# Kernel optimization log

Measured on AMD Instinct MI355X. Metric: run time of the kernel, lower is better.

## Reference

```python
import jax, jax.numpy as jnp
import numpy as np

BIT_DEPTH = 8  # feature squeezing

def setup_inputs() -> dict:
    key = jax.random.key(0)
    ks = jax.random.split(key, 8)
    B, C, H, W = 8, 256, 64, 64
    Cq = C // 8
    x = jax.random.normal(ks[0], (B, C, H, W), dtype=jnp.float32)
    # 1x1 conv weights stored as [out, in] (kernel dims squeezed)
    wq = jax.random.normal(ks[1], (Cq, C), dtype=jnp.float32) * 0.05
    bq = jax.random.normal(ks[2], (Cq,), dtype=jnp.float32) * 0.05
    wk = jax.random.normal(ks[3], (Cq, C), dtype=jnp.float32) * 0.05
    bk = jax.random.normal(ks[4], (Cq,), dtype=jnp.float32) * 0.05
    wv = jax.random.normal(ks[5], (C, C), dtype=jnp.float32) * 0.05
    bv = jax.random.normal(ks[6], (C,), dtype=jnp.float32) * 0.05
    gamma = jax.random.normal(ks[7], (1,), dtype=jnp.float32) * 0.1
    return {"x": x, "wq": wq, "bq": bq, "wk": wk, "bk": bk, "wv": wv, "bv": bv, "gamma": gamma}

def reference(x, wq, bq, wk, bk, wv, bv, gamma):
    B, C, H, W = x.shape
    N = H * W
    xf = x.reshape(B, C, N)  # flatten spatial
    # 1x1 convs == per-pixel linear projections
    q = jnp.einsum('bcn,oc->bon', xf, wq) + bq[None, :, None]   # [B, C/8, N]
    k = jnp.einsum('bcn,oc->bon', xf, wk) + bk[None, :, None]   # [B, C/8, N]
    v = jnp.einsum('bcn,oc->bon', xf, wv) + bv[None, :, None]   # [B, C, N]
    energy = jnp.einsum('bcn,bcm->bnm', q, k)                   # [B, N, N] (no scaling, as in source)
    attn = jax.nn.softmax(energy, axis=-1)
    out = jnp.einsum('bcm,bnm->bcn', v, attn).reshape(B, C, H, W)
    out = gamma[0] * out + out               # gamma-scaled residual of attention output
    scale = jnp.float32(2 ** BIT_DEPTH)
    return jnp.floor(out * scale) / scale    # feature squeezing (bit_depth=8)
```

## Files before the change

kernel.cpp:

```cpp
#include <hip/hip_runtime.h>
#include <math.h>

namespace {
constexpr int BB = 8;
constexpr int CH = 256;
constexpr int NN = 4096;
}

typedef float f32x4 __attribute__((ext_vector_type(4)));
typedef short bf16x8 __attribute__((ext_vector_type(8)));
typedef unsigned short us8 __attribute__((ext_vector_type(8)));

#define MFMA16(a, b, c) __builtin_amdgcn_mfma_f32_16x16x32_bf16(a, b, c, 0, 0, 0)

__device__ __forceinline__ unsigned short f2bf(float x) {
    unsigned int u = __float_as_uint(x);
    u += 0x7fffu + ((u >> 16) & 1u);
    return (unsigned short)(u >> 16);
}
__device__ __forceinline__ float bf2f(unsigned short h) {
    return __uint_as_float(((unsigned int)h) << 16);
}
__device__ __forceinline__ void gload16(const void* g, void* l) {
    __builtin_amdgcn_global_load_lds(
        (const __attribute__((address_space(1))) unsigned int*)g,
        (__attribute__((address_space(3))) unsigned int*)l, 16, 0, 0);
}

__global__ __launch_bounds__(256) void wsplit_kernel(
    const float* __restrict__ wq, const float* __restrict__ wk,
    const float* __restrict__ wv,
    unsigned short* __restrict__ wh, unsigned short* __restrict__ wl)
{
    int idx = blockIdx.x * 256 + threadIdx.x;
    float v;
    if (idx < 8192)       v = wq[idx];
    else if (idx < 16384) v = wk[idx - 8192];
    else                  v = wv[idx - 16384];
    unsigned short hi = f2bf(v);
    wh[idx] = hi;
    wl[idx] = f2bf(v - bf2f(hi));
}

#define PJ_XH 0
#define PJ_XL 32768
#define PJ_ST 65536
#define PJ_QK 65536
#define PJ_VE 0

__global__ __launch_bounds__(256, 2) void proj_kernel(
    const float* __restrict__ x,
    const unsigned short* __restrict__ wh, const unsigned short* __restrict__ wl,
    const float* __restrict__ bq, const float* __restrict__ bk,
    const float* __restrict__ bv,
    unsigned short* __restrict__ qh, unsigned short* __restrict__ ql,
    unsigned short* __restrict__ kh, unsigned short* __restrict__ kl,
    unsigned short* __restrict__ vt)
{
    __shared__ __align__(16) unsigned char smem[81920];
    const int t    = threadIdx.x;
    const int lane = t & 63;
    const int w    = t >> 6;
    const int l16  = lane & 15;
    const int quad = lane >> 4;
    const int b    = blockIdx.x >> 6;
    const int n0   = (blockIdx.x & 63) << 6;

    const unsigned char* xB = (const unsigned char*)x + ((size_t)b * 256 * NN + n0) * 4;
    const int n = t & 63;
    #pragma unroll 1
    for (int cg = 0; cg < 4; ++cg) {
        __syncthreads();
        #pragma unroll
        for (int j = 0; j < 4; ++j) {
            int idx = j * 256 + t;
            int cr = idx >> 4, nch = idx & 15;
            gload16(xB + (size_t)(cg * 64 + cr) * NN * 4 + nch * 16,
                    smem + PJ_ST + idx * 16);
        }
        __syncthreads();
        #pragma unroll
        for (int it = 0; it < 2; ++it) {
            int o = (t >> 6) + 4 * it;
            us8 h8, l8;
            #pragma unroll
            for (int j = 0; j < 8; ++j) {
                float v = *(const float*)(smem + PJ_ST + (o * 8 + j) * 256 + n * 4);
                unsigned short hi = f2bf(v);
                h8[j] = hi;
                l8[j] = f2bf(v - bf2f(hi));
            }
            int pch = (cg * 8 + o) ^ (n & 7);
            *(us8*)(smem + PJ_XH + n * 512 + pch * 16) = h8;
            *(us8*)(smem + PJ_XL + n * 512 + pch * 16) = l8;
        }
    }
    __syncthreads();

    f32x4 acc[5][4] = {};
    #pragma unroll 1
    for (int kc = 0; kc < 8; ++kc) {
        bf16x8 ah[5], al[5];
        #pragma unroll
        for (int i = 0; i < 5; ++i) {
            int och = (w * 5 + i) * 16 + l16;
            ah[i] = *(const bf16x8*)(wh + och * 256 + kc * 32 + quad * 8);
            al[i] = *(const bf16x8*)(wl + och * 256 + kc * 32 + quad * 8);
        }
        #pragma unroll
        for (int nt = 0; nt < 4; ++nt) {
            int roff = (nt * 16 + l16) * 512 + (((kc * 4 + quad) ^ (l16 & 7)) * 16);
            bf16x8 bh = *(const bf16x8*)(smem + PJ_XH + roff);
            bf16x8 bl = *(const bf16x8*)(smem + PJ_XL + roff);
            #pragma unroll
            for (int i = 0; i < 5; ++i) {
                acc[i][nt] = MFMA16(ah[i], bh, acc[i][nt]);
                acc[i][nt] = MFMA16(al[i], bh, acc[i][nt]);
                acc[i][nt] = MFMA16(ah[i], bl, acc[i][nt]);
            }
        }
    }
    __syncthreads();

    #pragma unroll
    for (int i = 0; i < 5; ++i) {
        int tile = w * 5 + i;
        if (tile < 4) {
            #pragma unroll
            for (int r = 0; r < 4; ++r) {
                int och = tile * 16 + quad * 4 + r;
                float bias = (och < 32) ? bq[och] : bk[och - 32];
                int arr = (och < 32) ? 0 : 2;
                int oq = och & 31;
                #pragma unroll
                for (int nt = 0; nt < 4; ++nt) {
                    float val = acc[i][nt][r] + bias;
                    unsigned short hi = f2bf(val);
                    unsigned short lo = f2bf(val - bf2f(hi));
                    *(unsigned short*)(smem + PJ_QK + arr * 4096 + (nt * 16 + l16) * 64 + oq * 2) = hi;
                    *(unsigned short*)(smem + PJ_QK + (arr + 1) * 4096 + (nt * 16 + l16) * 64 + oq * 2) = lo;
                }
            }
        } else {
            #pragma unroll
            for (int r = 0; r < 4; ++r) {
                int voch = tile * 16 + quad * 4 + r - 64;
                float bias = bv[voch];
                #pragma unroll
                for (int nt = 0; nt < 4; ++nt) {
                    *(unsigned short*)(smem + PJ_VE + voch * 136 + (nt * 16 + l16) * 2)
                        = f2bf(acc[i][nt][r] + bias);
                }
            }
        }
    }
    __syncthreads();

    {
        unsigned short* dsts[4] = { qh, ql, kh, kl };
        int arr = t >> 6, rn = t & 63;
        unsigned short* dst = dsts[arr] + ((size_t)b * NN + n0 + rn) * 32;
        #pragma unroll
        for (int i = 0; i < 4; ++i)
            *(us8*)(dst + i * 8) = *(const us8*)(smem + PJ_QK + arr * 4096 + rn * 64 + i * 16);
    }
    #pragma unroll
    for (int p = 0; p < 4; ++p) {
        int voch = p * 64 + (t >> 2), piece = t & 3;
        unsigned short* dst = vt + ((size_t)b * CH + voch) * NN + n0 + piece * 16;
        *(us8*)(dst)     = *(const us8*)(smem + PJ_VE + voch * 136 + piece * 32);
        *(us8*)(dst + 8) = *(const us8*)(smem + PJ_VE + voch * 136 + piece * 32 + 16);
    }
}

#define AV_OFF 0
#define AK_OFF 49152
#define AP_OFF 61440
#define AS_OFF 71680

__global__ __launch_bounds__(256, 2) void attn_kernel(
    const unsigned short* __restrict__ qh, const unsigned short* __restrict__ ql,
    const unsigned short* __restrict__ kh, const unsigned short* __restrict__ kl,
    const unsigned short* __restrict__ vt, const float* __restrict__ gptr,
    float* __restrict__ out)
{
    __shared__ __align__(16) unsigned char smem[71936];
    const int t    = threadIdx.x;
    const int lane = t & 63;
    const int w    = t >> 6;
    const int l16  = lane & 15;
    const int quad = lane >> 4;
    const int b    = blockIdx.x & 7;
    const int n0   = (blockIdx.x >> 3) << 6;

    const size_t qrow = (size_t)b * NN + n0 + w * 16 + l16;
    const bf16x8 qhA = *(const bf16x8*)(qh + qrow * 32 + quad * 8);
    const bf16x8 qlA = *(const bf16x8*)(ql + qrow * 32 + quad * 8);

    const unsigned char* ksrc;
    int kdst;
    {
        int c = t & 127, kr = c >> 2, cl = c & 3;
        int cg = cl ^ ((kr >> 1) & 3);
        ksrc = (const unsigned char*)((t < 128) ? kh : kl)
             + (size_t)b * NN * 64 + (size_t)kr * 64 + cg * 16;
        kdst = AK_OFF + (t >> 7) * 2048 + c * 16;
    }
    const unsigned char* vsrc;
    {
        int vr = t >> 2, cl = t & 3;
        int cg = cl ^ (vr & 3);
        vsrc = (const unsigned char*)vt + (size_t)b * CH * NN * 2
             + (size_t)vr * 8192 + cg * 16;
    }

    f32x4 acc[4][4] = {};
    float S[4] = {};

    {
        gload16(ksrc, smem + kdst);
        unsigned char* vd = smem + AV_OFF + t * 16;
        gload16(vsrc,           vd);
        gload16(vsrc + 524288,  vd + 4096);
        gload16(vsrc + 1048576, vd + 8192);
        gload16(vsrc + 1572864, vd + 12288);
    }
    __syncthreads();

    int bprv = 2, bcur = 0, bnxt = 1, pcur = 0;
    const int koffbase = (quad ^ ((l16 >> 1) & 3)) * 16;
    const int voffbase = (quad ^ (l16 & 3)) * 16;

    #pragma unroll 1
    for (int r = 0; r < 128; ++r) {
        if (r < 127) {
            const unsigned char* ks = ksrc + (size_t)(r + 1) * 2048;
            gload16(ks, smem + bnxt * 4096 + kdst);
            const unsigned char* vs = vsrc + (size_t)(r + 1) * 64;
            unsigned char* vd = smem + AV_OFF + bnxt * 16384 + t * 16;
            gload16(vs,           vd);
            gload16(vs + 524288,  vd + 4096);
            gload16(vs + 1048576, vd + 8192);
            gload16(vs + 1572864, vd + 12288);
        }
        {
            const unsigned char* kb = smem + AK_OFF + bcur * 4096;
            unsigned char* pb = smem + AP_OFF + pcur * 5120;
            #pragma unroll
            for (int kt = 0; kt < 2; ++kt) {
                int ko = (kt * 16 + l16) * 64 + koffbase;
                bf16x8 bh = *(const bf16x8*)(kb + ko);
                bf16x8 bl = *(const bf16x8*)(kb + 2048 + ko);
                f32x4 e = { 0.f, 0.f, 0.f, 0.f };
                e = MFMA16(qhA, bh, e);
                e = MFMA16(qlA, bh, e);
                e = MFMA16(qhA, bl, e);
                #pragma unroll
                for (int rr = 0; rr < 4; ++rr) {
                    float p = __expf(e[rr]);
                    unsigned short pv16 = f2bf(p);
                    S[rr] += bf2f(pv16);
                    *(unsigned short*)(pb + (w * 16 + quad * 4 + rr) * 80
                                          + (kt * 16 + l16) * 2) = pv16;
                }
            }
        }
        if (r > 0) {
            const unsigned char* pp = smem + AP_OFF + (pcur ^ 1) * 5120;
            const unsigned char* vb = smem + AV_OFF + bprv * 16384;
            bf16x8 aP[4], bV[4];
            #pragma unroll
            for (int qt = 0; qt < 4; ++qt)
                aP[qt] = *(const bf16x8*)(pp + (qt * 16 + l16) * 80 + quad * 16);
            #pragma unroll
            for (int ct = 0; ct < 4; ++ct)
                bV[ct] = *(const bf16x8*)(vb + (w * 64 + ct * 16 + l16) * 64 + voffbase);
            #pragma unroll
            for (int qt = 0; qt < 4; ++qt)
                #pragma unroll
                for (int ct = 0; ct < 4; ++ct)
                    acc[qt][ct] = MFMA16(aP[qt], bV[ct], acc[qt][ct]);
        }
        __syncthreads();
        bprv = bcur; bcur = bnxt; ++bnxt; if (bnxt == 3) bnxt = 0;
        pcur ^= 1;
    }
    {
        const unsigned char* pp = smem + AP_OFF + (pcur ^ 1) * 5120;
        const unsigned char* vb = smem + AV_OFF + bprv * 16384;
        bf16x8 aP[4], bV[4];
        #pragma unroll
        for (int qt = 0; qt < 4; ++qt)
            aP[qt] = *(const bf16x8*)(pp + (qt * 16 + l16) * 80 + quad * 16);
        #pragma unroll
        for (int ct = 0; ct < 4; ++ct)
            bV[ct] = *(const bf16x8*)(vb + (w * 64 + ct * 16 + l16) * 64 + voffbase);
        #pragma unroll
        for (int qt = 0; qt < 4; ++qt)
            #pragma unroll
            for (int ct = 0; ct < 4; ++ct)
                acc[qt][ct] = MFMA16(aP[qt], bV[ct], acc[qt][ct]);
    }

    #pragma unroll
    for (int mask = 1; mask <= 8; mask <<= 1)
        #pragma unroll
        for (int rr = 0; rr < 4; ++rr)
            S[rr] += __shfl_xor(S[rr], mask);
    float* SM = (float*)(smem + AS_OFF);
    __syncthreads();
    if (l16 == 0) {
        #pragma unroll
        for (int rr = 0; rr < 4; ++rr)
            SM[w * 16 + quad * 4 + rr] = S[rr];
    }
    __syncthreads();

    const float g1 = 1.f + gptr[0];
    float* ob = out + (size_t)b * CH * NN;
    #pragma unroll
    for (int qt = 0; qt < 4; ++qt) {
        float is[4];
        #pragma unroll
        for (int rr = 0; rr < 4; ++rr)
            is[rr] = g1 / SM[qt * 16 + quad * 4 + rr];
        #pragma unroll
        for (int ct = 0; ct < 4; ++ct) {
            float4 o4;
            o4.x = floorf(acc[qt][ct][0] * is[0] * 256.f) * 0.00390625f;
            o4.y = floorf(acc[qt][ct][1] * is[1] * 256.f) * 0.00390625f;
            o4.z = floorf(acc[qt][ct][2] * is[2] * 256.f) * 0.00390625f;
            o4.w = floorf(acc[qt][ct][3] * is[3] * 256.f) * 0.00390625f;
            *(float4*)(ob + (size_t)(w * 64 + ct * 16 + l16) * NN
                          + n0 + qt * 16 + quad * 4) = o4;
        }
    }
}

extern "C" void kernel_launch(void* const* d_in, const int* in_sizes, int n_in,
                              void* d_out, int out_size, void* d_ws, size_t ws_size,
                              hipStream_t stream) {
    const float* x  = (const float*)d_in[0];
    const float* wq = (const float*)d_in[1];
    const float* bq = (const float*)d_in[2];
    const float* wk = (const float*)d_in[3];
    const float* bk = (const float*)d_in[4];
    const float* wv = (const float*)d_in[5];
    const float* bv = (const float*)d_in[6];
    const float* gm = (const float*)d_in[7];
    float* out = (float*)d_out;

    unsigned short* ws = (unsigned short*)d_ws;
    const size_t WSZ = 320 * 256;
    const size_t QSZ = (size_t)BB * NN * 32;
    unsigned short* wh = ws;
    unsigned short* wl = wh + WSZ;
    unsigned short* qh = wl + WSZ;
    unsigned short* ql = qh + QSZ;
    unsigned short* kh = ql + QSZ;
    unsigned short* kl = kh + QSZ;
    unsigned short* vt = kl + QSZ;

    wsplit_kernel<<<320, 256, 0, stream>>>(wq, wk, wv, wh, wl);
    proj_kernel<<<512, 256, 0, stream>>>(x, wh, wl, bq, bk, bv,
                                         qh, ql, kh, kl, vt);
    attn_kernel<<<512, 256, 0, stream>>>(qh, ql, kh, kl, vt, gm, out);
}
```

Baseline: 246.9 us.

## Load K and V fragments straight to registers instead of staging through LDS

The attention kernel no longer copies K and V tiles into shared memory with async global-to-LDS loads. Each wave now reads its K fragment (16 keys) and V fragments directly from global memory into registers, double-buffered across iterations. Key tiles grow to 64 per iteration and each wave computes scores for all 64 queries, with partial row sums combined through shared memory at the end. The projection kernel likewise loads x with vectorized global reads into registers instead of LDS staging, shrinking shared memory. The intent is to cut LDS traffic and footprint to allow higher occupancy, at the cost of more registers and less coalesced, uncached direct global loads of V.

```diff
diff --git a/kernel.cpp b/kernel.cpp
--- a/kernel.cpp
+++ b/kernel.cpp
@@ -20,11 +20,6 @@
 }
 __device__ __forceinline__ float bf2f(unsigned short h) {
     return __uint_as_float(((unsigned int)h) << 16);
-}
-__device__ __forceinline__ void gload16(const void* g, void* l) {
-    __builtin_amdgcn_global_load_lds(
-        (const __attribute__((address_space(1))) unsigned int*)g,
-        (__attribute__((address_space(3))) unsigned int*)l, 16, 0, 0);
 }
 
 __global__ __launch_bounds__(256) void wsplit_kernel(
@@ -44,9 +39,8 @@
 
 #define PJ_XH 0
 #define PJ_XL 32768
-#define PJ_ST 65536
-#define PJ_QK 65536
 #define PJ_VE 0
+#define PJ_QK 36864
 
 __global__ __launch_bounds__(256, 2) void proj_kernel(
     const float* __restrict__ x,
@@ -57,7 +51,7 @@
     unsigned short* __restrict__ kh, unsigned short* __restrict__ kl,
     unsigned short* __restrict__ vt)
 {
-    __shared__ __align__(16) unsigned char smem[81920];
+    __shared__ __align__(16) unsigned char smem[65536];
     const int t    = threadIdx.x;
     const int lane = t & 63;
     const int w    = t >> 6;
@@ -66,33 +60,26 @@
     const int b    = blockIdx.x >> 6;
     const int n0   = (blockIdx.x & 63) << 6;
 
-    const unsigned char* xB = (const unsigned char*)x + ((size_t)b * 256 * NN + n0) * 4;
-    const int n = t & 63;
-    #pragma unroll 1
-    for (int cg = 0; cg < 4; ++cg) {
-        __syncthreads();
-        #pragma unroll
-        for (int j = 0; j < 4; ++j) {
-            int idx = j * 256 + t;
-            int cr = idx >> 4, nch = idx & 15;
-            gload16(xB + (size_t)(cg * 64 + cr) * NN * 4 + nch * 16,
-                    smem + PJ_ST + idx * 16);
-        }
-        __syncthreads();
-        #pragma unroll
-        for (int it = 0; it < 2; ++it) {
-            int o = (t >> 6) + 4 * it;
-            us8 h8, l8;
-            #pragma unroll
-            for (int j = 0; j < 8; ++j) {
-                float v = *(const float*)(smem + PJ_ST + (o * 8 + j) * 256 + n * 4);
-                unsigned short hi = f2bf(v);
-                h8[j] = hi;
-                l8[j] = f2bf(v - bf2f(hi));
-            }
-            int pch = (cg * 8 + o) ^ (n & 7);
-            *(us8*)(smem + PJ_XH + n * 512 + pch * 16) = h8;
-            *(us8*)(smem + PJ_XL + n * 512 + pch * 16) = l8;
+    const int cc = t & 15, pg = t >> 4;
+    const float* xg = x + (size_t)b * 256 * NN + n0 + pg * 4;
+    float4 xv[16];
+    #pragma unroll
+    for (int jc = 0; jc < 16; ++jc)
+        xv[jc] = *(const float4*)(xg + (size_t)(jc * 16 + cc) * NN);
+    #pragma unroll
+    for (int jc = 0; jc < 16; ++jc) {
+        const int c = jc * 16 + cc;
+        const int chunkb = c >> 3, cb = (c & 7) * 2;
+        #pragma unroll
+        for (int p = 0; p < 4; ++p) {
+            const int n = pg * 4 + p;
+            float v = (p == 0) ? xv[jc].x : (p == 1) ? xv[jc].y
+                    : (p == 2) ? xv[jc].z : xv[jc].w;
+            unsigned short hi = f2bf(v);
+            unsigned short lo = f2bf(v - bf2f(hi));
+            int off = n * 512 + ((chunkb ^ (n & 7)) * 16) + cb;
+            *(unsigned short*)(smem + PJ_XH + off) = hi;
+            *(unsigned short*)(smem + PJ_XL + off) = lo;
         }
     }
     __syncthreads();
@@ -173,10 +160,8 @@
     }
 }
 
-#define AV_OFF 0
-#define AK_OFF 49152
-#define AP_OFF 61440
-#define AS_OFF 71680
+#define AP_PAD 144
+#define AS_OFF 18432
 
 __global__ __launch_bounds__(256, 2) void attn_kernel(
     const unsigned short* __restrict__ qh, const unsigned short* __restrict__ ql,
@@ -184,7 +169,7 @@
     const unsigned short* __restrict__ vt, const float* __restrict__ gptr,
     float* __restrict__ out)
 {
-    __shared__ __align__(16) unsigned char smem[71936];
+    __shared__ __align__(16) unsigned char smem[19456];
     const int t    = threadIdx.x;
     const int lane = t & 63;
     const int w    = t >> 6;
@@ -193,126 +178,110 @@
     const int b    = blockIdx.x & 7;
     const int n0   = (blockIdx.x >> 3) << 6;
 
-    const size_t qrow = (size_t)b * NN + n0 + w * 16 + l16;
-    const bf16x8 qhA = *(const bf16x8*)(qh + qrow * 32 + quad * 8);
-    const bf16x8 qlA = *(const bf16x8*)(ql + qrow * 32 + quad * 8);
-
-    const unsigned char* ksrc;
-    int kdst;
-    {
-        int c = t & 127, kr = c >> 2, cl = c & 3;
-        int cg = cl ^ ((kr >> 1) & 3);
-        ksrc = (const unsigned char*)((t < 128) ? kh : kl)
-             + (size_t)b * NN * 64 + (size_t)kr * 64 + cg * 16;
-        kdst = AK_OFF + (t >> 7) * 2048 + c * 16;
-    }
-    const unsigned char* vsrc;
-    {
-        int vr = t >> 2, cl = t & 3;
-        int cg = cl ^ (vr & 3);
-        vsrc = (const unsigned char*)vt + (size_t)b * CH * NN * 2
-             + (size_t)vr * 8192 + cg * 16;
-    }
+    bf16x8 qhA[4], qlA[4];
+    #pragma unroll
+    for (int qt = 0; qt < 4; ++qt) {
+        size_t row = (size_t)b * NN + n0 + qt * 16 + l16;
+        qhA[qt] = *(const bf16x8*)(qh + row * 32 + quad * 8);
+        qlA[qt] = *(const bf16x8*)(ql + row * 32 + quad * 8);
+    }
+
+    const unsigned char* kp  = (const unsigned char*)kh
+        + ((size_t)b * NN + w * 16 + l16) * 64 + quad * 16;
+    const unsigned char* klp = (const unsigned char*)kl
+        + ((size_t)b * NN + w * 16 + l16) * 64 + quad * 16;
+    const unsigned char* vp  = (const unsigned char*)vt
+        + ((size_t)b * CH + w * 64 + l16) * (NN * 2) + quad * 16;
+
+    bf16x8 kfh[2], kfl[2], vf[2][8];
+    kfh[0] = *(const bf16x8*)kp;
+    kfl[0] = *(const bf16x8*)klp;
 
     f32x4 acc[4][4] = {};
-    float S[4] = {};
-
-    {
-        gload16(ksrc, smem + kdst);
-        unsigned char* vd = smem + AV_OFF + t * 16;
-        gload16(vsrc,           vd);
-        gload16(vsrc + 524288,  vd + 4096);
-        gload16(vsrc + 1048576, vd + 8192);
-        gload16(vsrc + 1572864, vd + 12288);
-    }
-    __syncthreads();
-
-    int bprv = 2, bcur = 0, bnxt = 1, pcur = 0;
-    const int koffbase = (quad ^ ((l16 >> 1) & 3)) * 16;
-    const int voffbase = (quad ^ (l16 & 3)) * 16;
-
-    #pragma unroll 1
-    for (int r = 0; r < 128; ++r) {
-        if (r < 127) {
-            const unsigned char* ks = ksrc + (size_t)(r + 1) * 2048;
-            gload16(ks, smem + bnxt * 4096 + kdst);
-            const unsigned char* vs = vsrc + (size_t)(r + 1) * 64;
-            unsigned char* vd = smem + AV_OFF + bnxt * 16384 + t * 16;
-            gload16(vs,           vd);
-            gload16(vs + 524288,  vd + 4096);
-            gload16(vs + 1048576, vd + 8192);
-            gload16(vs + 1572864, vd + 12288);
-        }
+    float S[4][4] = {};
+
+    #pragma unroll 2
+    for (int r = 0; r < 64; ++r) {
+        if (r < 63) {
+            kfh[(r + 1) & 1] = *(const bf16x8*)(kp  + (size_t)(r + 1) * 4096);
+            kfl[(r + 1) & 1] = *(const bf16x8*)(klp + (size_t)(r + 1) * 4096);
+        }
+        #pragma unroll
+        for (int ct = 0; ct < 4; ++ct)
+            #pragma unroll
+            for (int ks = 0; ks < 2; ++ks)
+                vf[r & 1][ct * 2 + ks] = *(const bf16x8*)
+                    (vp + (size_t)ct * 131072 + ks * 64 + (size_t)r * 128);
+
         {
-            const unsigned char* kb = smem + AK_OFF + bcur * 4096;
-            unsigned char* pb = smem + AP_OFF + pcur * 5120;
-            #pragma unroll
-            for (int kt = 0; kt < 2; ++kt) {
-                int ko = (kt * 16 + l16) * 64 + koffbase;
-                bf16x8 bh = *(const bf16x8*)(kb + ko);
-                bf16x8 bl = *(const bf16x8*)(kb + 2048 + ko);
+            unsigned char* pb = smem + (r & 1) * 9216;
+            const bf16x8 bh = kfh[r & 1], bl = kfl[r & 1];
+            #pragma unroll
+            for (int qt = 0; qt < 4; ++qt) {
                 f32x4 e = { 0.f, 0.f, 0.f, 0.f };
-                e = MFMA16(qhA, bh, e);
-                e = MFMA16(qlA, bh, e);
-                e = MFMA16(qhA, bl, e);
+                e = MFMA16(qhA[qt], bh, e);
+                e = MFMA16(qlA[qt], bh, e);
+                e = MFMA16(qhA[qt], bl, e);
                 #pragma unroll
                 for (int rr = 0; rr < 4; ++rr) {
                     float p = __expf(e[rr]);
                     unsigned short pv16 = f2bf(p);
-                    S[rr] += bf2f(pv16);
-                    *(unsigned short*)(pb + (w * 16 + quad * 4 + rr) * 80
-                                          + (kt * 16 + l16) * 2) = pv16;
+                    S[qt][rr] += bf2f(pv16);
+                    *(unsigned short*)(pb + (qt * 16 + quad * 4 + rr) * AP_PAD
+                                          + (w * 16 + l16) * 2) = pv16;
                 }
             }
         }
         if (r > 0) {
-            const unsigned char* pp = smem + AP_OFF + (pcur ^ 1) * 5120;
-            const unsigned char* vb = smem + AV_OFF + bprv * 16384;
-            bf16x8 aP[4], bV[4];
+            const unsigned char* pp = smem + ((r - 1) & 1) * 9216;
+            #pragma unroll
+            for (int ks = 0; ks < 2; ++ks) {
+                bf16x8 aP[4];
+                #pragma unroll
+                for (int qt = 0; qt < 4; ++qt)
+                    aP[qt] = *(const bf16x8*)(pp + (qt * 16 + l16) * AP_PAD
+                                                 + ks * 64 + quad * 16);
+                #pragma unroll
+                for (int qt = 0; qt < 4; ++qt)
+                    #pragma unroll
+                    for (int ct = 0; ct < 4; ++ct)
+                        acc[qt][ct] = MFMA16(aP[qt], vf[(r - 1) & 1][ct * 2 + ks],
+                                             acc[qt][ct]);
+            }
+        }
+        __syncthreads();
+    }
+    {
+        const unsigned char* pp = smem + 9216;
+        #pragma unroll
+        for (int ks = 0; ks < 2; ++ks) {
+            bf16x8 aP[4];
             #pragma unroll
             for (int qt = 0; qt < 4; ++qt)
-                aP[qt] = *(const bf16x8*)(pp + (qt * 16 + l16) * 80 + quad * 16);
-            #pragma unroll
-            for (int ct = 0; ct < 4; ++ct)
-                bV[ct] = *(const bf16x8*)(vb + (w * 64 + ct * 16 + l16) * 64 + voffbase);
+                aP[qt] = *(const bf16x8*)(pp + (qt * 16 + l16) * AP_PAD
+                                             + ks * 64 + quad * 16);
             #pragma unroll
             for (int qt = 0; qt < 4; ++qt)
                 #pragma unroll
                 for (int ct = 0; ct < 4; ++ct)
-                    acc[qt][ct] = MFMA16(aP[qt], bV[ct], acc[qt][ct]);
-        }
-        __syncthreads();
-        bprv = bcur; bcur = bnxt; ++bnxt; if (bnxt == 3) bnxt = 0;
-        pcur ^= 1;
-    }
-    {
-        const unsigned char* pp = smem + AP_OFF + (pcur ^ 1) * 5120;
-        const unsigned char* vb = smem + AV_OFF + bprv * 16384;
-        bf16x8 aP[4], bV[4];
+                    acc[qt][ct] = MFMA16(aP[qt], vf[1][ct * 2 + ks], acc[qt][ct]);
+        }
+    }
+
+    #pragma unroll
+    for (int mask = 1; mask <= 8; mask <<= 1)
         #pragma unroll
         for (int qt = 0; qt < 4; ++qt)
-            aP[qt] = *(const bf16x8*)(pp + (qt * 16 + l16) * 80 + quad * 16);
-        #pragma unroll
-        for (int ct = 0; ct < 4; ++ct)
-            bV[ct] = *(const bf16x8*)(vb + (w * 64 + ct * 16 + l16) * 64 + voffbase);
+            #pragma unroll
+            for (int rr = 0; rr < 4; ++rr)
+                S[qt][rr] += __shfl_xor(S[qt][rr], mask);
+    float* SM = (float*)(smem + AS_OFF);
+    if (l16 == 0) {
         #pragma unroll
         for (int qt = 0; qt < 4; ++qt)
             #pragma unroll
-            for (int ct = 0; ct < 4; ++ct)
-                acc[qt][ct] = MFMA16(aP[qt], bV[ct], acc[qt][ct]);
-    }
-
-    #pragma unroll
-    for (int mask = 1; mask <= 8; mask <<= 1)
-        #pragma unroll
-        for (int rr = 0; rr < 4; ++rr)
-            S[rr] += __shfl_xor(S[rr], mask);
-    float* SM = (float*)(smem + AS_OFF);
-    __syncthreads();
-    if (l16 == 0) {
-        #pragma unroll
-        for (int rr = 0; rr < 4; ++rr)
-            SM[w * 16 + quad * 4 + rr] = S[rr];
+            for (int rr = 0; rr < 4; ++rr)
+                SM[w * 64 + qt * 16 + quad * 4 + rr] = S[qt][rr];
     }
     __syncthreads();
 
@@ -322,8 +291,11 @@
     for (int qt = 0; qt < 4; ++qt) {
         float is[4];
         #pragma unroll
-        for (int rr = 0; rr < 4; ++rr)
-            is[rr] = g1 / SM[qt * 16 + quad * 4 + rr];
+        for (int rr = 0; rr < 4; ++rr) {
+            int qi = qt * 16 + quad * 4 + rr;
+            float Sf = SM[qi] + SM[64 + qi] + SM[128 + qi] + SM[192 + qi];
+            is[rr] = g1 / Sf;
+        }
         #pragma unroll
         for (int ct = 0; ct < 4; ++ct) {
             float4 o4;
```

Result: slower. 254.0 us (+2.9%).
